# Kernel optimization log

Hardware: AMD Instinct MI355X
Metric: run time of the kernel (lower is better)

Reference implementation:

```python
import jax, jax.numpy as jnp
import numpy as np

VOCAB = 50257
D_MODEL = 1024
PAD_IDX = 0
B, L = 4, 4096


def setup_inputs() -> dict:
    key = jax.random.key(0)
    k_emb, k_R, k_ids, k_role = jax.random.split(key, 4)
    emb = jax.random.normal(k_emb, (VOCAB, D_MODEL), dtype=jnp.float32)
    emb = emb.at[PAD_IDX].set(0.0)  # nn.Embedding padding_idx row is zero
    R = jax.random.normal(k_R, (D_MODEL, D_MODEL), dtype=jnp.float32)
    input_ids = jax.random.randint(k_ids, (B, L), 0, VOCAB, dtype=jnp.int64)
    role_mask = jax.random.randint(k_role, (B, L), 0, 2, dtype=jnp.int64)
    return {"input_ids": input_ids, "role_mask": role_mask, "emb": emb, "R": R}


def reference(input_ids, role_mask, emb, R):
    # embedding gather: (B, L, D)
    x = emb[input_ids]
    # agent tokens get x @ R.T, user tokens pass through
    agent = (role_mask == 1)[..., None]
    transformed = jnp.einsum('bld,ed->ble', x, R)
    return jnp.where(agent, transformed, x)
```

## Files before the change

### kernel.cpp

```cpp
#include <hip/hip_runtime.h>
#include <hip/hip_bf16.h>
#include <stdint.h>

#define DMODEL 1024
#define M_TOK  16384

typedef __attribute__((ext_vector_type(8))) short short8;
typedef __attribute__((ext_vector_type(4))) float f32x4;

__device__ __forceinline__ unsigned int pack2_bf16(float f0, float f1) {
    unsigned int u0 = __builtin_bit_cast(unsigned int, f0);
    unsigned int u1 = __builtin_bit_cast(unsigned int, f1);
    u0 += 0x7fffu + ((u0 >> 16) & 1u);
    u1 += 0x7fffu + ((u1 >> 16) & 1u);
    return __builtin_amdgcn_perm(u1, u0, 0x07060302);
}

__device__ __forceinline__ void gload_lds16(const void* g, void* l) {
    __builtin_amdgcn_global_load_lds(
        (const __attribute__((address_space(1))) void*)g,
        (__attribute__((address_space(3))) void*)l, 16, 0, 0);
}

__global__ void zero_ctr(int* __restrict__ n_agent) { *n_agent = 0; }

__global__ void __launch_bounds__(1024)
gather3(const int* __restrict__ ids, const int* __restrict__ roles,
        const float* __restrict__ emb, const float* __restrict__ Rm,
        __hip_bfloat16* __restrict__ Xc, __hip_bfloat16* __restrict__ Rb,
        float* __restrict__ out, int* __restrict__ orig,
        int* __restrict__ n_agent) {
    __shared__ int s_cnt[16];
    __shared__ int s_slot[16];
    const int wave = threadIdx.x >> 6;
    const int lane = threadIdx.x & 63;
    const int blk  = blockIdx.x;
    if (blk < M_TOK / 16) {
        const int row  = blk * 16 + wave;
        const int id   = ids[row];
        const int role = roles[row];
        if (lane == 0) s_cnt[wave] = (role == 1);
        __syncthreads();
        if (threadIdx.x == 0) {
            int tot = 0, pre[16];
#pragma unroll
            for (int w = 0; w < 16; ++w) { pre[w] = tot; tot += s_cnt[w]; }
            const int base = atomicAdd(n_agent, tot);
#pragma unroll
            for (int w = 0; w < 16; ++w) s_slot[w] = base + pre[w];
        }
        __syncthreads();
        const float* src = emb + (size_t)id * DMODEL;
        if (role == 1) {
            const int slot = s_slot[wave];
            if (lane == 0) orig[slot] = row;
            unsigned short* dst = (unsigned short*)(Xc + (size_t)slot * DMODEL);
#pragma unroll
            for (int c = 0; c < 4; ++c) {
                const int idx = c * 256 + lane * 4;
                float4 v = *(const float4*)(src + idx);
                uint2 p = make_uint2(pack2_bf16(v.x, v.y), pack2_bf16(v.z, v.w));
                *(uint2*)(dst + idx) = p;
            }
        } else {
            float* dst = out + (size_t)row * DMODEL;
#pragma unroll
            for (int c = 0; c < 4; ++c) {
                const int idx = c * 256 + lane * 4;
                *(float4*)(dst + idx) = *(const float4*)(src + idx);
            }
        }
    } else {
        const int r = (blk - M_TOK / 16) * 16 + wave;
        const float* src = Rm + (size_t)r * DMODEL;
        unsigned short* dst = (unsigned short*)(Rb + (size_t)r * DMODEL);
#pragma unroll
        for (int c = 0; c < 4; ++c) {
            const int idx = c * 256 + lane * 4;
            float4 v = *(const float4*)(src + idx);
            uint2 p = make_uint2(pack2_bf16(v.x, v.y), pack2_bf16(v.z, v.w));
            *(uint2*)(dst + idx) = p;
        }
    }
}

__global__ void __launch_bounds__(256)
rse_gemm4(const int* __restrict__ n_agent_p, const int* __restrict__ orig,
          const __hip_bfloat16* __restrict__ Xc,
          const __hip_bfloat16* __restrict__ Rb,
          float* __restrict__ out) {
    const int na = *n_agent_p;
    const int m0 = blockIdx.x * 128;
    if (m0 >= na) return;
    const int n0 = blockIdx.y * 128;

    __shared__ __hip_bfloat16 As[128 * 64];
    __shared__ __hip_bfloat16 Bs[128 * 64];
    __shared__ int s_orig[128];

    const int tid  = threadIdx.x;
    const int lane = tid & 63;
    const int wave = tid >> 6;
    const int quad = lane >> 4;
    const int l15  = lane & 15;
    const int wr   = wave >> 1;
    const int wc   = wave & 1;

    if (tid < 128) {
        const int j = m0 + tid;
        s_orig[tid] = (j < na) ? orig[j] : -1;
    }

    const int st_row = lane >> 3;
    const int st_k   = ((lane & 7) ^ st_row) * 8;
    const __hip_bfloat16* aG = Xc + (size_t)m0 * DMODEL + st_k;
    const __hip_bfloat16* bG = Rb + (size_t)n0 * DMODEL + st_k;

    f32x4 acc[4][4] = {};

    for (int k0 = 0; k0 < DMODEL; k0 += 64) {
        __syncthreads();
#pragma unroll
        for (int q = 0; q < 4; ++q) {
            const int rg = (q * 4 + wave) * 8;
            gload_lds16(aG + (size_t)(rg + st_row) * DMODEL + k0, &As[rg * 64]);
            gload_lds16(bG + (size_t)(rg + st_row) * DMODEL + k0, &Bs[rg * 64]);
        }
        __syncthreads();

#pragma unroll
        for (int kk = 0; kk < 2; ++kk) {
            short8 af[4], bfr[4];
#pragma unroll
            for (int i = 0; i < 4; ++i) {
                const int r = wr * 64 + i * 16 + l15;
                af[i] = *(const short8*)&As[r * 64 + ((kk * 4 + quad) ^ (r & 7)) * 8];
            }
#pragma unroll
            for (int j = 0; j < 4; ++j) {
                const int r = wc * 64 + j * 16 + l15;
                bfr[j] = *(const short8*)&Bs[r * 64 + ((kk * 4 + quad) ^ (r & 7)) * 8];
            }
#pragma unroll
            for (int i = 0; i < 4; ++i)
#pragma unroll
                for (int j = 0; j < 4; ++j)
                    acc[i][j] = __builtin_amdgcn_mfma_f32_16x16x32_bf16(af[i], bfr[j], acc[i][j], 0, 0, 0);
        }
    }

    const int colbase = n0 + wc * 64 + l15;
#pragma unroll
    for (int ti = 0; ti < 4; ++ti) {
        const int rowb = wr * 64 + ti * 16 + quad * 4;
#pragma unroll
        for (int r = 0; r < 4; ++r) {
            const int oj = s_orig[rowb + r];
            if (oj >= 0) {
                float* dst = out + (size_t)oj * DMODEL + colbase;
#pragma unroll
                for (int tj = 0; tj < 4; ++tj)
                    dst[tj * 16] = acc[ti][tj][r];
            }
        }
    }
}

extern "C" void kernel_launch(void* const* d_in, const int* in_sizes, int n_in,
                              void* d_out, int out_size, void* d_ws, size_t ws_size,
                              hipStream_t stream) {
    const int*   ids   = (const int*)d_in[0];
    const int*   roles = (const int*)d_in[1];
    const float* emb   = (const float*)d_in[2];
    const float* Rm    = (const float*)d_in[3];
    float*       out   = (float*)d_out;

    __hip_bfloat16* Xc = (__hip_bfloat16*)d_ws;
    __hip_bfloat16* Rb = Xc + (size_t)M_TOK * DMODEL;
    int* orig    = (int*)(Rb + (size_t)DMODEL * DMODEL);
    int* n_agent = orig + M_TOK;

    zero_ctr<<<1, 1, 0, stream>>>(n_agent);
    gather3<<<M_TOK / 16 + DMODEL / 16, 1024, 0, stream>>>(
        ids, roles, emb, Rm, Xc, Rb, out, orig, n_agent);
    dim3 grid2(M_TOK / 128, DMODEL / 128);
    rse_gemm4<<<grid2, 256, 0, stream>>>(n_agent, orig, Xc, Rb, out);
}
```

Before: 309.8 us.

## Double-buffer LDS in GEMM and shrink M tile to 64 rows

The GEMM now uses two LDS buffers, so the async global-to-LDS load of the next K slice is issued before computing on the current one. This removes one barrier per K step and hides load latency behind the MFMA work. The M tile is also halved to 64 rows, doubling the block count, which gives more parallelism and less wasted work in the last partial tile. In exchange, each block reuses the B tile across fewer rows, so more global and L2 traffic goes to loading R.

```diff
diff --git a/kernel.cpp b/kernel.cpp
--- a/kernel.cpp
+++ b/kernel.cpp
@@ -85,18 +85,18 @@
 }
 
 __global__ void __launch_bounds__(256)
-rse_gemm4(const int* __restrict__ n_agent_p, const int* __restrict__ orig,
+rse_gemm5(const int* __restrict__ n_agent_p, const int* __restrict__ orig,
           const __hip_bfloat16* __restrict__ Xc,
           const __hip_bfloat16* __restrict__ Rb,
           float* __restrict__ out) {
     const int na = *n_agent_p;
-    const int m0 = blockIdx.x * 128;
+    const int m0 = blockIdx.x * 64;
     if (m0 >= na) return;
     const int n0 = blockIdx.y * 128;
 
-    __shared__ __hip_bfloat16 As[128 * 64];
-    __shared__ __hip_bfloat16 Bs[128 * 64];
-    __shared__ int s_orig[128];
+    __shared__ __hip_bfloat16 As[2][64 * 64];
+    __shared__ __hip_bfloat16 Bs[2][128 * 64];
+    __shared__ int s_orig[64];
 
     const int tid  = threadIdx.x;
     const int lane = tid & 63;
@@ -106,7 +106,7 @@
     const int wr   = wave >> 1;
     const int wc   = wave & 1;
 
-    if (tid < 128) {
+    if (tid < 64) {
         const int j = m0 + tid;
         s_orig[tid] = (j < na) ? orig[j] : -1;
     }
@@ -116,51 +116,76 @@
     const __hip_bfloat16* aG = Xc + (size_t)m0 * DMODEL + st_k;
     const __hip_bfloat16* bG = Rb + (size_t)n0 * DMODEL + st_k;
 
-    f32x4 acc[4][4] = {};
-
-    for (int k0 = 0; k0 < DMODEL; k0 += 64) {
-        __syncthreads();
-#pragma unroll
-        for (int q = 0; q < 4; ++q) {
-            const int rg = (q * 4 + wave) * 8;
-            gload_lds16(aG + (size_t)(rg + st_row) * DMODEL + k0, &As[rg * 64]);
-            gload_lds16(bG + (size_t)(rg + st_row) * DMODEL + k0, &Bs[rg * 64]);
-        }
-        __syncthreads();
-
-#pragma unroll
-        for (int kk = 0; kk < 2; ++kk) {
-            short8 af[4], bfr[4];
-#pragma unroll
-            for (int i = 0; i < 4; ++i) {
-                const int r = wr * 64 + i * 16 + l15;
-                af[i] = *(const short8*)&As[r * 64 + ((kk * 4 + quad) ^ (r & 7)) * 8];
-            }
-#pragma unroll
-            for (int j = 0; j < 4; ++j) {
-                const int r = wc * 64 + j * 16 + l15;
-                bfr[j] = *(const short8*)&Bs[r * 64 + ((kk * 4 + quad) ^ (r & 7)) * 8];
-            }
-#pragma unroll
-            for (int i = 0; i < 4; ++i)
-#pragma unroll
-                for (int j = 0; j < 4; ++j)
-                    acc[i][j] = __builtin_amdgcn_mfma_f32_16x16x32_bf16(af[i], bfr[j], acc[i][j], 0, 0, 0);
-        }
-    }
+#define STAGE(buf, k0)                                                        \
+    do {                                                                      \
+        _Pragma("unroll")                                                     \
+        for (int q = 0; q < 2; ++q) {         \
+            const int rg = (q * 4 + wave) * 8;                                \
+            gload_lds16(aG + (size_t)(rg + st_row) * DMODEL + (k0),           \
+                        &As[buf][rg * 64]);                                   \
+        }                                                                     \
+        _Pragma("unroll")                                                     \
+        for (int q = 0; q < 4; ++q) {        \
+            const int rg = (q * 4 + wave) * 8;                                \
+            gload_lds16(bG + (size_t)(rg + st_row) * DMODEL + (k0),           \
+                        &Bs[buf][rg * 64]);                                   \
+        }                                                                     \
+    } while (0)
+
+    f32x4 acc[2][4] = {};
+
+#define COMPUTE(buf)                                                          \
+    do {                                                                      \
+        _Pragma("unroll")                                                     \
+        for (int kk = 0; kk < 2; ++kk) {                                      \
+            short8 af[2], bfr[4];                                             \
+            _Pragma("unroll")                                                 \
+            for (int i = 0; i < 2; ++i) {                                     \
+                const int r = wr * 32 + i * 16 + l15;                         \
+                af[i] = *(const short8*)                                      \
+                    &As[buf][r * 64 + ((kk * 4 + quad) ^ (r & 7)) * 8];       \
+            }                                                                 \
+            _Pragma("unroll")                                                 \
+            for (int j = 0; j < 4; ++j) {                                     \
+                const int r = wc * 64 + j * 16 + l15;                         \
+                bfr[j] = *(const short8*)                                     \
+                    &Bs[buf][r * 64 + ((kk * 4 + quad) ^ (r & 7)) * 8];       \
+            }                                                                 \
+            _Pragma("unroll")                                                 \
+            for (int i = 0; i < 2; ++i)                                       \
+                _Pragma("unroll")                                             \
+                for (int j = 0; j < 4; ++j)                                   \
+                    acc[i][j] = __builtin_amdgcn_mfma_f32_16x16x32_bf16(      \
+                        af[i], bfr[j], acc[i][j], 0, 0, 0);                   \
+        }                                                                     \
+    } while (0)
+
+    STAGE(0, 0);
+    __syncthreads();
+
+    for (int k0 = 0; k0 < DMODEL; k0 += 128) {
+        STAGE(1, k0 + 64);
+        COMPUTE(0);
+        __syncthreads();
+        if (k0 + 128 < DMODEL) STAGE(0, k0 + 128);
+        COMPUTE(1);
+        __syncthreads();
+    }
+#undef STAGE
+#undef COMPUTE
 
     const int colbase = n0 + wc * 64 + l15;
 #pragma unroll
-    for (int ti = 0; ti < 4; ++ti) {
-        const int rowb = wr * 64 + ti * 16 + quad * 4;
+    for (int i = 0; i < 2; ++i) {
+        const int rowb = wr * 32 + i * 16 + quad * 4;
 #pragma unroll
         for (int r = 0; r < 4; ++r) {
             const int oj = s_orig[rowb + r];
             if (oj >= 0) {
                 float* dst = out + (size_t)oj * DMODEL + colbase;
 #pragma unroll
-                for (int tj = 0; tj < 4; ++tj)
-                    dst[tj * 16] = acc[ti][tj][r];
+                for (int j = 0; j < 4; ++j)
+                    dst[j * 16] = acc[i][j][r];
             }
         }
     }
@@ -183,6 +208,6 @@
     zero_ctr<<<1, 1, 0, stream>>>(n_agent);
     gather3<<<M_TOK / 16 + DMODEL / 16, 1024, 0, stream>>>(
         ids, roles, emb, Rm, Xc, Rb, out, orig, n_agent);
-    dim3 grid2(M_TOK / 128, DMODEL / 128);
-    rse_gemm4<<<grid2, 256, 0, stream>>>(n_agent, orig, Xc, Rb, out);
-}
+    dim3 grid2(M_TOK / 64, DMODEL / 128);
+    rse_gemm5<<<grid2, 256, 0, stream>>>(n_agent, orig, Xc, Rb, out);
+}
```

Result: no change. 314.8 us (+1.6%).
